# Kernel tuning notes

Measured on AMD Instinct MI355X. Metric: run time of the kernel, lower is better.

## Reference

```python
import jax, jax.numpy as jnp
import numpy as np

B, D, K, N = 32, 512, 64, 1024
EPS = 1e-12  # torch F.normalize eps


def setup_inputs() -> dict:
    key = jax.random.key(0)
    k1, k2, k3 = jax.random.split(key, 3)
    x = jax.random.normal(k1, (B, D, N), dtype=jnp.float32)
    conv_w = jax.random.normal(k2, (K, D), dtype=jnp.float32) * (1.0 / np.sqrt(D))
    centers = jax.random.normal(k3, (D, K), dtype=jnp.float32)
    return {"x": x, "conv_w": conv_w, "centers": centers}


def reference(x, conv_w, centers):
    # scores: 1x1 conv over flattened spatial dim -> [B, K, N]
    scores = jnp.einsum('kd,bdn->bkn', conv_w, x)
    assign = jax.nn.softmax(scores, axis=1)                 # softmax over clusters
    # Algebraic rewrite of sum_n assign[b,k,n] * (x[b,d,n] - centers[d,k]):
    vlad = (jnp.einsum('bdn,bkn->bdk', x, assign)
            - centers[None, :, :] * assign.sum(axis=-1)[:, None, :])  # [B, D, K]
    # intra-normalization over descriptor dim D (F.normalize with eps clamp)
    vlad = vlad / jnp.maximum(jnp.linalg.norm(vlad, axis=1, keepdims=True), EPS)
    desc = vlad.reshape(vlad.shape[0], -1)                  # [B, D*K]
    desc = desc / jnp.maximum(jnp.linalg.norm(desc, axis=1, keepdims=True), EPS)
    return desc
```

## Files before the change

### kernel.cpp

```cpp
#include <hip/hip_runtime.h>
#include <hip/hip_bf16.h>

#define Bv 32
#define Dv 512
#define Kv 64
#define Nv 1024
#define EPSv 1e-12f

typedef __attribute__((ext_vector_type(8))) short bf16x8;
typedef __attribute__((ext_vector_type(4))) float f32x4;

__device__ __forceinline__ unsigned short f2b(float f) {
  union { float f; unsigned u; } v; v.f = f;
  unsigned r = v.u + 0x7fffu + ((v.u >> 16) & 1u);
  return (unsigned short)(r >> 16);
}
__device__ __forceinline__ unsigned pack2(float a, float b) {
  return (unsigned)f2b(a) | ((unsigned)f2b(b) << 16);
}

#define GLOAD_LDS16(gsrc, ldst)                                             \
  __builtin_amdgcn_global_load_lds(                                         \
      (const __attribute__((address_space(1))) void*)(gsrc),                \
      (__attribute__((address_space(3))) void*)(ldst), 16, 0, 0)

__global__ __launch_bounds__(256) void wconv(const float* __restrict__ w,
                                             unsigned short* __restrict__ wbf,
                                             float* __restrict__ zbuf) {
  int id = blockIdx.x * 256 + threadIdx.x;
  int i = id * 4;
  float4 v = *(const float4*)&w[i];
  uint2 o = make_uint2(pack2(v.x, v.y), pack2(v.z, v.w));
  *(uint2*)&wbf[i] = o;
  if (id < 2 * Bv * Kv) zbuf[id] = 0.f;
}

__global__ __launch_bounds__(512) void fused_scores(
    const float* __restrict__ x, const unsigned short* __restrict__ wbf,
    unsigned short* __restrict__ xbf, unsigned short* __restrict__ assign,
    float* __restrict__ asum) {
  __shared__ unsigned short xT[64 * 520];
  __shared__ float redmax[4][64];
  __shared__ float redsum[4][64];

  const int t = threadIdx.x;
  const int flat = blockIdx.x;
  const int i0 = flat >> 3;
  const int b = (flat & 7) + 8 * (i0 & 3);
  const int nt = i0 >> 2;
  const int n0 = nt * 64;

  {
    const int lo = t & 15;
    const int hi = t >> 4;
    const int s = (lo >> 1) & 3;
    const float* xb = x + (size_t)b * Dv * Nv + n0;
    unsigned short* xt = xbf + ((size_t)b * 16 + nt) * (Dv * 64);
#pragma unroll
    for (int r = 0; r < 8; r++) {
      int d = (hi + 32 * r) * 2;
      int n4 = lo * 4;
      float4 v0 = *(const float4*)&xb[(size_t)d * Nv + n4];
      float4 v1 = *(const float4*)&xb[(size_t)(d + 1) * Nv + n4];
      *(uint2*)&xt[(size_t)d * 64 + n4] =
          make_uint2(pack2(v0.x, v0.y), pack2(v0.z, v0.w));
      *(uint2*)&xt[(size_t)(d + 1) * 64 + n4] =
          make_uint2(pack2(v1.x, v1.y), pack2(v1.z, v1.w));
      unsigned w0 = pack2(v0.x, v1.x);
      unsigned w1 = pack2(v0.y, v1.y);
      unsigned w2 = pack2(v0.z, v1.z);
      unsigned w3 = pack2(v0.w, v1.w);
      unsigned a0 = (s & 1) ? w1 : w0, a1 = (s & 1) ? w2 : w1,
               a2 = (s & 1) ? w3 : w2, a3 = (s & 1) ? w0 : w3;
      unsigned b0 = (s & 2) ? a2 : a0, b1 = (s & 2) ? a3 : a1,
               b2 = (s & 2) ? a0 : a2, b3 = (s & 2) ? a1 : a3;
      *(unsigned*)&xT[(n4 + ((0 + s) & 3)) * 520 + d] = b0;
      *(unsigned*)&xT[(n4 + ((1 + s) & 3)) * 520 + d] = b1;
      *(unsigned*)&xT[(n4 + ((2 + s) & 3)) * 520 + d] = b2;
      *(unsigned*)&xT[(n4 + ((3 + s) & 3)) * 520 + d] = b3;
    }
  }
  __syncthreads();

  const int wv = t >> 6;
  const int lane = t & 63;
  const int q = lane >> 4;
  const int m = lane & 15;
  const int k16 = wv & 3;
  const int nsub = wv >> 2;

  f32x4 acc0 = {0.f, 0.f, 0.f, 0.f};
  f32x4 acc1 = {0.f, 0.f, 0.f, 0.f};

  const unsigned short* wp = wbf + (size_t)(k16 * 16 + m) * Dv + q * 8;
  const unsigned short* l0 = &xT[(nsub * 32 + m) * 520 + q * 8];
  const unsigned short* l1 = l0 + 16 * 520;

#pragma unroll
  for (int d0 = 0; d0 < Dv; d0 += 32) {
    bf16x8 af = *(const bf16x8*)(wp + d0);
    bf16x8 bf0 = *(const bf16x8*)(l0 + d0);
    bf16x8 bf1 = *(const bf16x8*)(l1 + d0);
    acc0 = __builtin_amdgcn_mfma_f32_16x16x32_bf16(af, bf0, acc0, 0, 0, 0);
    acc1 = __builtin_amdgcn_mfma_f32_16x16x32_bf16(af, bf1, acc1, 0, 0, 0);
  }

  float m0 = fmaxf(fmaxf(acc0[0], acc0[1]), fmaxf(acc0[2], acc0[3]));
  float m1 = fmaxf(fmaxf(acc1[0], acc1[1]), fmaxf(acc1[2], acc1[3]));
  m0 = fmaxf(m0, __shfl_xor(m0, 16)); m0 = fmaxf(m0, __shfl_xor(m0, 32));
  m1 = fmaxf(m1, __shfl_xor(m1, 16)); m1 = fmaxf(m1, __shfl_xor(m1, 32));
  if (q == 0) {
    redmax[k16][nsub * 32 + m] = m0;
    redmax[k16][nsub * 32 + 16 + m] = m1;
  }
  __syncthreads();
  const int c0 = nsub * 32 + m, c1 = c0 + 16;
  float mc0 = fmaxf(fmaxf(redmax[0][c0], redmax[1][c0]), fmaxf(redmax[2][c0], redmax[3][c0]));
  float mc1 = fmaxf(fmaxf(redmax[0][c1], redmax[1][c1]), fmaxf(redmax[2][c1], redmax[3][c1]));

  float e0[4], e1[4];
  float s0 = 0.f, s1 = 0.f;
#pragma unroll
  for (int r = 0; r < 4; r++) {
    e0[r] = __expf(acc0[r] - mc0); s0 += e0[r];
    e1[r] = __expf(acc1[r] - mc1); s1 += e1[r];
  }
  s0 += __shfl_xor(s0, 16); s0 += __shfl_xor(s0, 32);
  s1 += __shfl_xor(s1, 16); s1 += __shfl_xor(s1, 32);
  if (q == 0) {
    redsum[k16][c0] = s0;
    redsum[k16][c1] = s1;
  }
  __syncthreads();
  float sc0 = 1.0f / (redsum[0][c0] + redsum[1][c0] + redsum[2][c0] + redsum[3][c0]);
  float sc1 = 1.0f / (redsum[0][c1] + redsum[1][c1] + redsum[2][c1] + redsum[3][c1]);

  unsigned short* at_ = assign + ((size_t)b * 16 + nt) * (Kv * 64)
                        + (size_t)(k16 * 16 + q * 4) * 64 + nsub * 32;
#pragma unroll
  for (int r = 0; r < 4; r++) {
    float v0 = e0[r] * sc0;
    float v1 = e1[r] * sc1;
    at_[r * 64 + m] = f2b(v0);
    at_[r * 64 + 16 + m] = f2b(v1);
    float p = v0 + v1;
    p += __shfl_xor(p, 1); p += __shfl_xor(p, 2);
    p += __shfl_xor(p, 4); p += __shfl_xor(p, 8);
    if (m == 0) atomicAdd(&asum[b * Kv + k16 * 16 + q * 4 + r], p);
  }
}

__global__ __launch_bounds__(256) void vlad_stage(
    const unsigned short* __restrict__ xbf, const unsigned short* __restrict__ assign,
    const float* __restrict__ centers, const float* __restrict__ asum,
    float* __restrict__ vlad, float* __restrict__ colsq) {
  __shared__ unsigned short xs[2][2 * 2048];
  __shared__ unsigned short as_[2][2 * 4096];

  const int t = threadIdx.x;
  const int flat = blockIdx.x;
  const int i0 = flat >> 3;
  const int b = (flat & 7) + 8 * (i0 & 3);
  const int dg = i0 >> 2;

  const int w = t >> 6;
  const int dh = w & 1;
  const int kh = w >> 1;
  const int lane = t & 63;
  const int q = lane >> 4;
  const int m = lane & 15;

  const int rs = lane >> 3;
  const int csw = (lane & 7) ^ (rs & 7);

  const unsigned short* xbase = xbf + (size_t)b * 16 * (Dv * 64) + dg * 2048;
  const unsigned short* abase = assign + (size_t)b * 16 * (Kv * 64);

#define STAGE(buf, rr)                                                        \
  {                                                                           \
    _Pragma("unroll")                                                         \
    for (int s = 0; s < 2; s++) {                                             \
      int tile = (rr) * 2 + s;                                                \
      const unsigned short* _xs = xbase + (size_t)tile * (Dv * 64)            \
                                  + (w * 8 + rs) * 64 + csw * 8;              \
      const unsigned short* _a1 = abase + (size_t)tile * (Kv * 64)            \
                                  + (w * 16 + rs) * 64 + csw * 8;             \
      GLOAD_LDS16(_xs, &xs[buf][s * 2048 + w * 512]);                         \
      GLOAD_LDS16(_a1, &as_[buf][s * 4096 + w * 1024]);                       \
      GLOAD_LDS16(_a1 + 512, &as_[buf][s * 4096 + w * 1024 + 512]);           \
    }                                                                         \
  }

  f32x4 acc0 = {0.f,0.f,0.f,0.f}, acc1 = {0.f,0.f,0.f,0.f};

  STAGE(0, 0)
  asm volatile("s_waitcnt vmcnt(0)");
  __syncthreads();

  int buf = 0;
#pragma unroll
  for (int rr = 0; rr < 8; rr++) {
    if (rr < 7) STAGE(buf ^ 1, rr + 1)
#pragma unroll
    for (int s = 0; s < 2; s++) {
#pragma unroll
      for (int nc = 0; nc < 2; nc++) {
        const int cidx = (((nc * 4 + q) ^ (m & 7))) * 8;
        bf16x8 xv = *(const bf16x8*)&xs[buf][s * 2048 + (dh * 16 + m) * 64 + cidx];
        bf16x8 a0 = *(const bf16x8*)&as_[buf][s * 4096 + (kh * 32 + m) * 64 + cidx];
        bf16x8 a1 = *(const bf16x8*)&as_[buf][s * 4096 + (kh * 32 + 16 + m) * 64 + cidx];
        acc0 = __builtin_amdgcn_mfma_f32_16x16x32_bf16(xv, a0, acc0, 0, 0, 0);
        acc1 = __builtin_amdgcn_mfma_f32_16x16x32_bf16(xv, a1, acc1, 0, 0, 0);
      }
    }
    asm volatile("s_waitcnt vmcnt(0)");
    __syncthreads();
    buf ^= 1;
  }
#undef STAGE

  const int k0 = kh * 32 + m;
  const int k1 = k0 + 16;
  const float as0 = asum[b * Kv + k0];
  const float as1 = asum[b * Kv + k1];
  float ss0 = 0.f, ss1 = 0.f;
#pragma unroll
  for (int r = 0; r < 4; r++) {
    int d = dg * 32 + dh * 16 + q * 4 + r;
    float v0 = acc0[r] - centers[d * Kv + k0] * as0;
    float v1 = acc1[r] - centers[d * Kv + k1] * as1;
    vlad[((size_t)b * Dv + d) * Kv + k0] = v0;
    vlad[((size_t)b * Dv + d) * Kv + k1] = v1;
    ss0 = fmaf(v0, v0, ss0);
    ss1 = fmaf(v1, v1, ss1);
  }
  ss0 += __shfl_xor(ss0, 16); ss0 += __shfl_xor(ss0, 32);
  ss1 += __shfl_xor(ss1, 16); ss1 += __shfl_xor(ss1, 32);
  if (q == 0) {
    atomicAdd(&colsq[b * Kv + k0], ss0);
    atomicAdd(&colsq[b * Kv + k1], ss1);
  }
}

__global__ __launch_bounds__(256) void scale_kernel(
    const float* __restrict__ vlad, const float* __restrict__ colsq,
    float* __restrict__ out) {
  const int t = threadIdx.x;
  const size_t i = ((size_t)blockIdx.x * 256 + t) * 4;
  const int b = (int)(i >> 15);
  __shared__ float scs[64];
  __shared__ float bsh;
  if (t < 64) {
    float tot = colsq[b * Kv + t];
    float sc = 1.0f / fmaxf(sqrtf(tot), EPSv);
    scs[t] = sc;
    float contrib = tot * sc * sc;
#pragma unroll
    for (int off = 32; off > 0; off >>= 1) contrib += __shfl_down(contrib, off);
    if (t == 0) bsh = 1.0f / fmaxf(sqrtf(contrib), EPSv);
  }
  __syncthreads();
  float4 v = *(const float4*)&vlad[i];
  const int k = (int)(i & 63);
  float4 o;
  o.x = v.x * scs[k + 0] * bsh;
  o.y = v.y * scs[k + 1] * bsh;
  o.z = v.z * scs[k + 2] * bsh;
  o.w = v.w * scs[k + 3] * bsh;
  *(float4*)&out[i] = o;
}

extern "C" void kernel_launch(void* const* d_in, const int* in_sizes, int n_in,
                              void* d_out, int out_size, void* d_ws, size_t ws_size,
                              hipStream_t stream) {
  const float* x = (const float*)d_in[0];
  const float* w = (const float*)d_in[1];
  const float* centers = (const float*)d_in[2];
  float* out = (float*)d_out;

  char* ws = (char*)d_ws;
  unsigned short* assign = (unsigned short*)ws;
  float* vlad = (float*)(ws + 4194304);
  unsigned short* xbf = (unsigned short*)(ws + 8388608);
  unsigned short* wbf = (unsigned short*)(ws + 41943040);
  float* asum = (float*)(ws + 42008576);
  float* colsq = asum + Bv * Kv;

  wconv<<<32, 256, 0, stream>>>(w, wbf, asum);
  fused_scores<<<512, 512, 0, stream>>>(x, wbf, xbf, assign, asum);
  vlad_stage<<<512, 256, 0, stream>>>(xbf, assign, centers, asum, vlad, colsq);
  scale_kernel<<<1024, 256, 0, stream>>>(vlad, colsq, out);
}
```

Baseline: 124.6 us.

## Drop bf16 x copy; read fp32 x directly in vlad stage and convert in-register

The scores kernel no longer writes a tiled bf16 copy of x to workspace. The vlad stage instead streams the original fp32 x into LDS with a swizzled layout and converts it to bf16 with v_cvt_pk_bf16_f32 just before the MFMA. This removes a 32 MB write from the first kernel but doubles the bytes the second kernel reads for x (64 MB fp32 vs 32 MB bf16), which may be served partly from cache. LDS usage and conversion ALU work in the inner loop also go up.

```diff
diff --git a/kernel.cpp b/kernel.cpp
--- a/kernel.cpp
+++ b/kernel.cpp
@@ -17,6 +17,11 @@
 }
 __device__ __forceinline__ unsigned pack2(float a, float b) {
   return (unsigned)f2b(a) | ((unsigned)f2b(b) << 16);
+}
+__device__ __forceinline__ unsigned cvtpk(float a, float b) {
+  unsigned r;
+  asm("v_cvt_pk_bf16_f32 %0, %1, %2" : "=v"(r) : "v"(a), "v"(b));
+  return r;
 }
 
 #define GLOAD_LDS16(gsrc, ldst)                                             \
@@ -37,8 +42,7 @@
 
 __global__ __launch_bounds__(512) void fused_scores(
     const float* __restrict__ x, const unsigned short* __restrict__ wbf,
-    unsigned short* __restrict__ xbf, unsigned short* __restrict__ assign,
-    float* __restrict__ asum) {
+    unsigned short* __restrict__ assign, float* __restrict__ asum) {
   __shared__ unsigned short xT[64 * 520];
   __shared__ float redmax[4][64];
   __shared__ float redsum[4][64];
@@ -55,17 +59,12 @@
     const int hi = t >> 4;
     const int s = (lo >> 1) & 3;
     const float* xb = x + (size_t)b * Dv * Nv + n0;
-    unsigned short* xt = xbf + ((size_t)b * 16 + nt) * (Dv * 64);
 #pragma unroll
     for (int r = 0; r < 8; r++) {
       int d = (hi + 32 * r) * 2;
       int n4 = lo * 4;
       float4 v0 = *(const float4*)&xb[(size_t)d * Nv + n4];
       float4 v1 = *(const float4*)&xb[(size_t)(d + 1) * Nv + n4];
-      *(uint2*)&xt[(size_t)d * 64 + n4] =
-          make_uint2(pack2(v0.x, v0.y), pack2(v0.z, v0.w));
-      *(uint2*)&xt[(size_t)(d + 1) * 64 + n4] =
-          make_uint2(pack2(v1.x, v1.y), pack2(v1.z, v1.w));
       unsigned w0 = pack2(v0.x, v1.x);
       unsigned w1 = pack2(v0.y, v1.y);
       unsigned w2 = pack2(v0.z, v1.z);
@@ -151,11 +150,11 @@
 }
 
 __global__ __launch_bounds__(256) void vlad_stage(
-    const unsigned short* __restrict__ xbf, const unsigned short* __restrict__ assign,
+    const float* __restrict__ x, const unsigned short* __restrict__ assign,
     const float* __restrict__ centers, const float* __restrict__ asum,
     float* __restrict__ vlad, float* __restrict__ colsq) {
-  __shared__ unsigned short xs[2][2 * 2048];
-  __shared__ unsigned short as_[2][2 * 4096];
+  __shared__ float xsf[2][2][2048];
+  __shared__ unsigned short as_[2][2][4096];
 
   const int t = threadIdx.x;
   const int flat = blockIdx.x;
@@ -171,9 +170,10 @@
   const int m = lane & 15;
 
   const int rs = lane >> 3;
-  const int csw = (lane & 7) ^ (rs & 7);
-
-  const unsigned short* xbase = xbf + (size_t)b * 16 * (Dv * 64) + dg * 2048;
+  const int csw_a = (lane & 7) ^ (rs & 7);
+  const int rx = lane >> 4;
+
+  const float* xdg = x + ((size_t)b * Dv + dg * 32) * Nv;
   const unsigned short* abase = assign + (size_t)b * 16 * (Kv * 64);
 
 #define STAGE(buf, rr)                                                        \
@@ -181,13 +181,17 @@
     _Pragma("unroll")                                                         \
     for (int s = 0; s < 2; s++) {                                             \
       int tile = (rr) * 2 + s;                                                \
-      const unsigned short* _xs = xbase + (size_t)tile * (Dv * 64)            \
-                                  + (w * 8 + rs) * 64 + csw * 8;              \
+      _Pragma("unroll")                                                       \
+      for (int i = 0; i < 2; i++) {                                           \
+        int dl = w * 8 + i * 4 + rx;                   \
+        const float* _xs = xdg + (size_t)dl * Nv + tile * 64                  \
+                           + (((lane & 15) ^ (dl & 7)) * 4);                  \
+        GLOAD_LDS16(_xs, &xsf[buf][s][(w * 8 + i * 4) * 64]);                 \
+      }                                                                       \
       const unsigned short* _a1 = abase + (size_t)tile * (Kv * 64)            \
-                                  + (w * 16 + rs) * 64 + csw * 8;             \
-      GLOAD_LDS16(_xs, &xs[buf][s * 2048 + w * 512]);                         \
-      GLOAD_LDS16(_a1, &as_[buf][s * 4096 + w * 1024]);                       \
-      GLOAD_LDS16(_a1 + 512, &as_[buf][s * 4096 + w * 1024 + 512]);           \
+                                  + (w * 16 + rs) * 64 + csw_a * 8;           \
+      GLOAD_LDS16(_a1, &as_[buf][s][w * 1024]);                               \
+      GLOAD_LDS16(_a1 + 512, &as_[buf][s][w * 1024 + 512]);                   \
     }                                                                         \
   }
 
@@ -198,6 +202,8 @@
   __syncthreads();
 
   int buf = 0;
+  const int row = dh * 16 + m;
+  const int mk7 = m & 7;
 #pragma unroll
   for (int rr = 0; rr < 8; rr++) {
     if (rr < 7) STAGE(buf ^ 1, rr + 1)
@@ -205,10 +211,18 @@
     for (int s = 0; s < 2; s++) {
 #pragma unroll
       for (int nc = 0; nc < 2; nc++) {
-        const int cidx = (((nc * 4 + q) ^ (m & 7))) * 8;
-        bf16x8 xv = *(const bf16x8*)&xs[buf][s * 2048 + (dh * 16 + m) * 64 + cidx];
-        bf16x8 a0 = *(const bf16x8*)&as_[buf][s * 4096 + (kh * 32 + m) * 64 + cidx];
-        bf16x8 a1 = *(const bf16x8*)&as_[buf][s * 4096 + (kh * 32 + 16 + m) * 64 + cidx];
+        const int c0 = nc * 8 + q * 2;
+        float4 f0 = *(const float4*)&xsf[buf][s][row * 64 + ((c0 ^ mk7)) * 4];
+        float4 f1 = *(const float4*)&xsf[buf][s][row * 64 + (((c0 + 1) ^ mk7)) * 4];
+        bf16x8 xv;
+        unsigned* xu = (unsigned*)&xv;
+        xu[0] = cvtpk(f0.x, f0.y);
+        xu[1] = cvtpk(f0.z, f0.w);
+        xu[2] = cvtpk(f1.x, f1.y);
+        xu[3] = cvtpk(f1.z, f1.w);
+        const int cidx = ((nc * 4 + q) ^ mk7) * 8;
+        bf16x8 a0 = *(const bf16x8*)&as_[buf][s][(kh * 32 + m) * 64 + cidx];
+        bf16x8 a1 = *(const bf16x8*)&as_[buf][s][(kh * 32 + 16 + m) * 64 + cidx];
         acc0 = __builtin_amdgcn_mfma_f32_16x16x32_bf16(xv, a0, acc0, 0, 0, 0);
         acc1 = __builtin_amdgcn_mfma_f32_16x16x32_bf16(xv, a1, acc1, 0, 0, 0);
       }
@@ -281,13 +295,12 @@
   char* ws = (char*)d_ws;
   unsigned short* assign = (unsigned short*)ws;
   float* vlad = (float*)(ws + 4194304);
-  unsigned short* xbf = (unsigned short*)(ws + 8388608);
-  unsigned short* wbf = (unsigned short*)(ws + 41943040);
-  float* asum = (float*)(ws + 42008576);
+  unsigned short* wbf = (unsigned short*)(ws + 8388608);
+  float* asum = (float*)(ws + 8454144);
   float* colsq = asum + Bv * Kv;
 
   wconv<<<32, 256, 0, stream>>>(w, wbf, asum);
-  fused_scores<<<512, 512, 0, stream>>>(x, wbf, xbf, assign, asum);
-  vlad_stage<<<512, 256, 0, stream>>>(xbf, assign, centers, asum, vlad, colsq);
+  fused_scores<<<512, 512, 0, stream>>>(x, wbf, assign, asum);
+  vlad_stage<<<512, 256, 0, stream>>>(x, assign, centers, asum, vlad, colsq);
   scale_kernel<<<1024, 256, 0, stream>>>(vlad, colsq, out);
 }
```

After: 123.6 us. No clear change (-0.8%).
